# Kernel optimization log

Measured on AMD Instinct MI355X. Metric: run time of the kernel, lower is better.

Reference implementation:

```python
import jax, jax.numpy as jnp
import numpy as np

BANDWIDTH = 0.1
NUM_ITERS = 5


def setup_inputs() -> dict:
    key = jax.random.key(0)
    # image batch in [0,1], BCHW
    x = jax.random.uniform(key, (2, 3, 96, 96), dtype=jnp.float32)
    return {"x": x}


def reference(x):
    # Mean-shift filtering: each pixel feature y is iteratively moved to the
    # Gaussian-kernel weighted mean of ALL original pixel features:
    #   y_{t+1} = sum_j exp(-||y_t - x_j||^2 / (2 bw^2)) x_j / sum_j exp(...)
    B, C, H, W = x.shape
    N = H * W
    pts = x.reshape(B, C, N).transpose(0, 2, 1)  # [B, N, C] original points
    inv2bw2 = jnp.float32(1.0 / (2.0 * BANDWIDTH * BANDWIDTH))
    x_sq = jnp.sum(pts * pts, axis=-1)  # [B, N]

    def step(y, _):
        # squared pairwise distances via ||y||^2 + ||x||^2 - 2 y.x  -> [B, N, N]
        y_sq = jnp.sum(y * y, axis=-1)  # [B, N]
        d2 = y_sq[:, :, None] + x_sq[:, None, :] - 2.0 * jnp.einsum(
            'bnc,bmc->bnm', y, pts)
        w = jnp.exp(-jnp.maximum(d2, 0.0) * inv2bw2)  # Gaussian kernel weights
        num = jnp.einsum('bnm,bmc->bnc', w, pts)  # weighted sum of points
        den = jnp.sum(w, axis=-1, keepdims=True)  # normalizer (>= 1, self-weight)
        return num / den, None

    y, _ = jax.lax.scan(step, pts, None, length=NUM_ITERS)
    return y.transpose(0, 2, 1).reshape(B, C, H, W)
```

## Files before the change

kernel.cpp:

```cpp
#include <hip/hip_runtime.h>
#include <math.h>


typedef float v2f __attribute__((ext_vector_type(2)));

#define NPTS   9216
#define NB     2
#define TOT    (NB * NPTS)
#define MSPLIT 32
#define SLICE  (NPTS / MSPLIT)
#define WSLICE (SLICE / 4)
#define NPB    256
#define NTILES (NPTS / NPB)
#define LOG2E  1.44269504088896340736f

__device__ __forceinline__ v2f splat2(float v) { return (v2f){v, v}; }


__global__ __launch_bounds__(256, 4) void ms_iter(const float* __restrict__ x,
                                                  const float4* __restrict__ accIn,
                                                  float4* __restrict__ accOut,
                                                  float s, int first) {
    __shared__ float4 smem[1024];
    float* const xs = (float*)smem;
    float* const ys = xs + SLICE;
    float* const zs = ys + SLICE;
    float* const ws = zs + SLICE;
    float4* const ypar = smem + SLICE;
    float4* const red  = smem;

    const int tid  = threadIdx.x;
    const int lane = tid & 63;
    const int wv   = tid >> 6;
    const int k    = blockIdx.x % MSPLIT;
    const int tile = blockIdx.x / MSPLIT;
    const int b    = tile / NTILES;
    const int nt   = tile - b * NTILES;
    const int nbase = nt * NPB;
    const float* xb = x + b * 3 * NPTS;
    const int mbeg = k * SLICE;

    for (int i = tid; i < SLICE; i += 256) {
        int g = mbeg + i;
        float px = xb[g] * s;
        float py = xb[NPTS + g] * s;
        float pz = xb[2 * NPTS + g] * s;
        xs[i] = 2.f * px;
        ys[i] = 2.f * py;
        zs[i] = 2.f * pz;
        ws[i] = -fmaf(px, px, fmaf(py, py, pz * pz));
    }
    {
        float y0, y1, y2;
        if (first) {
            int n = nbase + tid;
            y0 = xb[n] * s; y1 = xb[NPTS + n] * s; y2 = xb[2 * NPTS + n] * s;
        } else {
            float4 a = accIn[b * NPTS + nbase + tid];
            float inv = 1.0f / a.w;
            y0 = a.x * inv; y1 = a.y * inv; y2 = a.z * inv;
        }
        ypar[tid] = make_float4(y0, y1, y2,
                                -fmaf(y0, y0, fmaf(y1, y1, y2 * y2)));
    }
    __syncthreads();

    v2f Yx[4], Yy[4], Yz[4], Yw[4], Ax[4], Ay[4], Az[4], Aw[4];
#pragma unroll
    for (int j = 0; j < 4; ++j) {
        float4 yp = ypar[lane + 64 * j];
        Yx[j] = splat2(yp.x); Yy[j] = splat2(yp.y);
        Yz[j] = splat2(yp.z); Yw[j] = splat2(yp.w);
        Ax[j] = splat2(0.f); Ay[j] = splat2(0.f);
        Az[j] = splat2(0.f); Aw[j] = splat2(0.f);
    }

    const float* xsw = xs + wv * WSLICE;
    const float* ysw = ys + wv * WSLICE;
    const float* zsw = zs + wv * WSLICE;
    const float* wsw = ws + wv * WSLICE;

    for (int i = 0; i < WSLICE; i += 8) {
#pragma unroll
        for (int half = 0; half < 2; ++half) {
            const int o = i + 4 * half;
            float4 PX = *(const float4*)(xsw + o);
            float4 PY = *(const float4*)(ysw + o);
            float4 PZ = *(const float4*)(zsw + o);
            float4 PW = *(const float4*)(wsw + o);
            v2f px0 = (v2f){PX.x, PX.y}, px1 = (v2f){PX.z, PX.w};
            v2f py0 = (v2f){PY.x, PY.y}, py1 = (v2f){PY.z, PY.w};
            v2f pz0 = (v2f){PZ.x, PZ.y}, pz1 = (v2f){PZ.z, PZ.w};
            v2f pw0 = (v2f){PW.x, PW.y}, pw1 = (v2f){PW.z, PW.w};
#pragma unroll
            for (int j = 0; j < 4; ++j) {
                v2f t0 = pw0 + Yw[j];
                t0 = __builtin_elementwise_fma(pz0, Yz[j], t0);
                t0 = __builtin_elementwise_fma(py0, Yy[j], t0);
                t0 = __builtin_elementwise_fma(px0, Yx[j], t0);
                v2f t1 = pw1 + Yw[j];
                t1 = __builtin_elementwise_fma(pz1, Yz[j], t1);
                t1 = __builtin_elementwise_fma(py1, Yy[j], t1);
                t1 = __builtin_elementwise_fma(px1, Yx[j], t1);
                v2f w0, w1;
                w0.x = __builtin_amdgcn_exp2f(t0.x);
                w0.y = __builtin_amdgcn_exp2f(t0.y);
                w1.x = __builtin_amdgcn_exp2f(t1.x);
                w1.y = __builtin_amdgcn_exp2f(t1.y);
                Ax[j] = __builtin_elementwise_fma(w0, px0, Ax[j]);
                Ay[j] = __builtin_elementwise_fma(w0, py0, Ay[j]);
                Az[j] = __builtin_elementwise_fma(w0, pz0, Az[j]);
                Aw[j] += w0;
                Ax[j] = __builtin_elementwise_fma(w1, px1, Ax[j]);
                Ay[j] = __builtin_elementwise_fma(w1, py1, Ay[j]);
                Az[j] = __builtin_elementwise_fma(w1, pz1, Az[j]);
                Aw[j] += w1;
            }
        }
    }

    __syncthreads();
#pragma unroll
    for (int j = 0; j < 4; ++j) {
        red[wv * NPB + lane + 64 * j] =
            make_float4(Ax[j].x + Ax[j].y, Ay[j].x + Ay[j].y,
                        Az[j].x + Az[j].y, Aw[j].x + Aw[j].y);
    }
    __syncthreads();
    {
        float4 r0 = red[tid];
        float4 r1 = red[NPB + tid];
        float4 r2 = red[2 * NPB + tid];
        float4 r3 = red[3 * NPB + tid];
        float ox = 0.5f * ((r0.x + r1.x) + (r2.x + r3.x));
        float oy = 0.5f * ((r0.y + r1.y) + (r2.y + r3.y));
        float oz = 0.5f * ((r0.z + r1.z) + (r2.z + r3.z));
        float od = (r0.w + r1.w) + (r2.w + r3.w);
        float* dst = (float*)&accOut[b * NPTS + nbase + tid];
        atomicAdd(dst + 0, ox);
        atomicAdd(dst + 1, oy);
        atomicAdd(dst + 2, oz);
        atomicAdd(dst + 3, od);
    }
}

__global__ __launch_bounds__(256) void ms_pack(const float4* __restrict__ acc4,
                                               float* __restrict__ out,
                                               float invs) {
    int gid = blockIdx.x * 256 + threadIdx.x;
    int b = gid / NPTS;
    int n = gid - b * NPTS;
    float4 a = acc4[gid];
    float f = invs / a.w;
    float* ob = out + b * 3 * NPTS;
    ob[n]            = a.x * f;
    ob[NPTS + n]     = a.y * f;
    ob[2 * NPTS + n] = a.z * f;
}

extern "C" void kernel_launch(void* const* d_in, const int* in_sizes, int n_in,
                              void* d_out, int out_size, void* d_ws, size_t ws_size,
                              hipStream_t stream) {
    const float* x = (const float*)d_in[0];
    float* out = (float*)d_out;
    float s = sqrtf(50.0f * LOG2E);

    float4* acc = (float4*)d_ws;

    hipMemsetAsync(acc, 0, (size_t)5 * TOT * sizeof(float4), stream);

    for (int it = 0; it < 5; ++it) {
        const float4* accIn = (it == 0) ? nullptr : acc + (size_t)(it - 1) * TOT;
        ms_iter<<<NB * NTILES * MSPLIT, 256, 0, stream>>>(
            x, accIn, acc + (size_t)it * TOT, s, it == 0 ? 1 : 0);
    }
    ms_pack<<<TOT / 256, 256, 0, stream>>>(acc + (size_t)4 * TOT, out, 1.0f / s);
}
```

Baseline: 235.0 us.

## Compute pairwise distance logits with split-bf16 MFMA instead of scalar FMAs

The pairwise dot products plus norm terms are moved onto the 32x32x16 bf16 MFMA. Each feature is split into hi and lo bf16 parts so the products keep close to fp32 accuracy. A new pre-pass kernel packs the point features into bf16 layout and float4 points once, and each wave streams points from global memory instead of staging them in LDS. The exp and weighted accumulation stay on the vector ALU, and the result is reduced across half-waves with a shuffle before the atomics. The risk is precision loss from the bf16 splitting, and the kernel now relies more on global memory and cache bandwidth.

```diff
diff --git a/kernel.cpp b/kernel.cpp
--- a/kernel.cpp
+++ b/kernel.cpp
@@ -2,145 +2,154 @@
 #include <math.h>
 
 
+#define NPTS 9216
+#define NB 2
+#define TOT (NB * NPTS)
+#define NTIL 288
+#define TPW 18
+#define LOG2E 1.44269504088896340736f
+
 typedef float v2f __attribute__((ext_vector_type(2)));
+typedef short bf16x8 __attribute__((ext_vector_type(8)));
+typedef float f32x16 __attribute__((ext_vector_type(16)));
 
-#define NPTS   9216
-#define NB     2
-#define TOT    (NB * NPTS)
-#define MSPLIT 32
-#define SLICE  (NPTS / MSPLIT)
-#define WSLICE (SLICE / 4)
-#define NPB    256
-#define NTILES (NPTS / NPB)
-#define LOG2E  1.44269504088896340736f
+__device__ __forceinline__ unsigned short bf16r(float x) {
+    unsigned u = __float_as_uint(x);
+    return (unsigned short)((u + 0x7fffu + ((u >> 16) & 1u)) >> 16);
+}
+__device__ __forceinline__ float bf16f(unsigned short h) {
+    return __uint_as_float((unsigned)h << 16);
+}
 
-__device__ __forceinline__ v2f splat2(float v) { return (v2f){v, v}; }
+__global__ __launch_bounds__(256) void ms_feat(const float* __restrict__ x,
+                                               short* __restrict__ pfeat,
+                                               float4* __restrict__ pts4,
+                                               float s) {
+    int gid = blockIdx.x * 256 + threadIdx.x;
+    int b = gid / NPTS, m = gid - b * NPTS;
+    const float* xb = x + b * 3 * NPTS;
+    float p0 = xb[m] * s, p1 = xb[NPTS + m] * s, p2 = xb[2 * NPTS + m] * s;
+    float np = -fmaf(p0, p0, fmaf(p1, p1, p2 * p2));
+    float a0 = 2.f * p0, a1 = 2.f * p1, a2 = 2.f * p2;
+    unsigned short Ah0 = bf16r(a0), Ah1 = bf16r(a1), Ah2 = bf16r(a2);
+    unsigned short Al0 = bf16r(a0 - bf16f(Ah0));
+    unsigned short Al1 = bf16r(a1 - bf16f(Ah1));
+    unsigned short Al2 = bf16r(a2 - bf16f(Ah2));
+    unsigned short Nh = bf16r(np);
+    unsigned short Nl = bf16r(np - bf16f(Nh));
+    uint4* dst = (uint4*)(pfeat + (size_t)gid * 16);
+    dst[0] = make_uint4((unsigned)Ah0 | ((unsigned)Ah1 << 16),
+                        (unsigned)Ah2 | ((unsigned)Ah0 << 16),
+                        (unsigned)Ah1 | ((unsigned)Ah2 << 16),
+                        (unsigned)Al0 | ((unsigned)Al1 << 16));
+    dst[1] = make_uint4((unsigned)Al2 | ((unsigned)Al0 << 16),
+                        (unsigned)Al1 | ((unsigned)Al2 << 16),
+                        (unsigned)Nh  | ((unsigned)Nl  << 16), 0u);
+    pts4[gid] = make_float4(p0, p1, p2, 1.0f);
+}
 
+__global__ __launch_bounds__(256, 4) void ms_iter(
+    const float* __restrict__ x, const float4* __restrict__ accIn,
+    float4* __restrict__ accOut, const short* __restrict__ pfeat,
+    const float4* __restrict__ pts4, float s, int first) {
 
-__global__ __launch_bounds__(256, 4) void ms_iter(const float* __restrict__ x,
-                                                  const float4* __restrict__ accIn,
-                                                  float4* __restrict__ accOut,
-                                                  float s, int first) {
-    __shared__ float4 smem[1024];
-    float* const xs = (float*)smem;
-    float* const ys = xs + SLICE;
-    float* const zs = ys + SLICE;
-    float* const ws = zs + SLICE;
-    float4* const ypar = smem + SLICE;
-    float4* const red  = smem;
+    const int tid = threadIdx.x;
+    const int l   = tid & 63;
+    const int wv  = tid >> 6;
+    const int col = l & 31;
+    const int hi  = l >> 5;
 
-    const int tid  = threadIdx.x;
-    const int lane = tid & 63;
-    const int wv   = tid >> 6;
-    const int k    = blockIdx.x % MSPLIT;
-    const int tile = blockIdx.x / MSPLIT;
-    const int b    = tile / NTILES;
-    const int nt   = tile - b * NTILES;
-    const int nbase = nt * NPB;
-    const float* xb = x + b * 3 * NPTS;
-    const int mbeg = k * SLICE;
+    int bid = blockIdx.x;
+    const int b  = bid / (4 * NTIL);
+    int r        = bid - b * 4 * NTIL;
+    const int nt = r >> 2;
+    const int mc = r & 3;
+    const int n  = nt * 32 + col;
+    const int t0 = (mc * 4 + wv) * TPW;
 
-    for (int i = tid; i < SLICE; i += 256) {
-        int g = mbeg + i;
-        float px = xb[g] * s;
-        float py = xb[NPTS + g] * s;
-        float pz = xb[2 * NPTS + g] * s;
-        xs[i] = 2.f * px;
-        ys[i] = 2.f * py;
-        zs[i] = 2.f * pz;
-        ws[i] = -fmaf(px, px, fmaf(py, py, pz * pz));
+    float y0, y1, y2;
+    if (first) {
+        const float* xb = x + b * 3 * NPTS;
+        y0 = xb[n] * s; y1 = xb[NPTS + n] * s; y2 = xb[2 * NPTS + n] * s;
+    } else {
+        float4 a = accIn[b * NPTS + n];
+        float inv = 1.0f / a.w;
+        y0 = a.x * inv; y1 = a.y * inv; y2 = a.z * inv;
     }
-    {
-        float y0, y1, y2;
-        if (first) {
-            int n = nbase + tid;
-            y0 = xb[n] * s; y1 = xb[NPTS + n] * s; y2 = xb[2 * NPTS + n] * s;
-        } else {
-            float4 a = accIn[b * NPTS + nbase + tid];
-            float inv = 1.0f / a.w;
-            y0 = a.x * inv; y1 = a.y * inv; y2 = a.z * inv;
-        }
-        ypar[tid] = make_float4(y0, y1, y2,
-                                -fmaf(y0, y0, fmaf(y1, y1, y2 * y2)));
-    }
-    __syncthreads();
-
-    v2f Yx[4], Yy[4], Yz[4], Yw[4], Ax[4], Ay[4], Az[4], Aw[4];
-#pragma unroll
-    for (int j = 0; j < 4; ++j) {
-        float4 yp = ypar[lane + 64 * j];
-        Yx[j] = splat2(yp.x); Yy[j] = splat2(yp.y);
-        Yz[j] = splat2(yp.z); Yw[j] = splat2(yp.w);
-        Ax[j] = splat2(0.f); Ay[j] = splat2(0.f);
-        Az[j] = splat2(0.f); Aw[j] = splat2(0.f);
+    float ny = -fmaf(y0, y0, fmaf(y1, y1, y2 * y2));
+    unsigned short Yh0 = bf16r(y0), Yh1 = bf16r(y1), Yh2 = bf16r(y2);
+    unsigned short Yl0 = bf16r(y0 - bf16f(Yh0));
+    unsigned short Yl1 = bf16r(y1 - bf16f(Yh1));
+    unsigned short Yl2 = bf16r(y2 - bf16f(Yh2));
+    union { unsigned w[4]; bf16x8 v; } yf;
+    if (hi == 0) {
+        yf.w[0] = (unsigned)Yh0 | ((unsigned)Yh1 << 16);
+        yf.w[1] = (unsigned)Yh2 | ((unsigned)Yl0 << 16);
+        yf.w[2] = (unsigned)Yl1 | ((unsigned)Yl2 << 16);
+        yf.w[3] = (unsigned)Yh0 | ((unsigned)Yh1 << 16);
+    } else {
+        yf.w[0] = (unsigned)Yh2 | ((unsigned)Yl0 << 16);
+        yf.w[1] = (unsigned)Yl1 | ((unsigned)Yl2 << 16);
+        yf.w[2] = 0x3F803F80u;
+        yf.w[3] = 0u;
     }
 
-    const float* xsw = xs + wv * WSLICE;
-    const float* ysw = ys + wv * WSLICE;
-    const float* zsw = zs + wv * WSLICE;
-    const float* wsw = ws + wv * WSLICE;
+    f32x16 cin;
+#pragma unroll
+    for (int i = 0; i < 16; ++i) cin[i] = ny;
 
-    for (int i = 0; i < WSLICE; i += 8) {
+    v2f Axy = (v2f){0.f, 0.f};
+    v2f Azw = (v2f){0.f, 0.f};
+
+    const short*  pfb = pfeat + (size_t)b * NPTS * 16;
+    const float4* pbb = pts4 + (size_t)b * NPTS + 4 * hi;
+
+#pragma unroll 2
+    for (int t = t0; t < t0 + TPW; ++t) {
+        const int m0 = t * 32;
+        bf16x8 pf = *(const bf16x8*)(pfb + (size_t)(m0 + col) * 16 + 8 * hi);
+        f32x16 u = __builtin_amdgcn_mfma_f32_32x32x16_bf16(pf, yf.v, cin,
+                                                           0, 0, 0);
+        const float4* pb = pbb + m0;
 #pragma unroll
-        for (int half = 0; half < 2; ++half) {
-            const int o = i + 4 * half;
-            float4 PX = *(const float4*)(xsw + o);
-            float4 PY = *(const float4*)(ysw + o);
-            float4 PZ = *(const float4*)(zsw + o);
-            float4 PW = *(const float4*)(wsw + o);
-            v2f px0 = (v2f){PX.x, PX.y}, px1 = (v2f){PX.z, PX.w};
-            v2f py0 = (v2f){PY.x, PY.y}, py1 = (v2f){PY.z, PY.w};
-            v2f pz0 = (v2f){PZ.x, PZ.y}, pz1 = (v2f){PZ.z, PZ.w};
-            v2f pw0 = (v2f){PW.x, PW.y}, pw1 = (v2f){PW.z, PW.w};
-#pragma unroll
-            for (int j = 0; j < 4; ++j) {
-                v2f t0 = pw0 + Yw[j];
-                t0 = __builtin_elementwise_fma(pz0, Yz[j], t0);
-                t0 = __builtin_elementwise_fma(py0, Yy[j], t0);
-                t0 = __builtin_elementwise_fma(px0, Yx[j], t0);
-                v2f t1 = pw1 + Yw[j];
-                t1 = __builtin_elementwise_fma(pz1, Yz[j], t1);
-                t1 = __builtin_elementwise_fma(py1, Yy[j], t1);
-                t1 = __builtin_elementwise_fma(px1, Yx[j], t1);
-                v2f w0, w1;
-                w0.x = __builtin_amdgcn_exp2f(t0.x);
-                w0.y = __builtin_amdgcn_exp2f(t0.y);
-                w1.x = __builtin_amdgcn_exp2f(t1.x);
-                w1.y = __builtin_amdgcn_exp2f(t1.y);
-                Ax[j] = __builtin_elementwise_fma(w0, px0, Ax[j]);
-                Ay[j] = __builtin_elementwise_fma(w0, py0, Ay[j]);
-                Az[j] = __builtin_elementwise_fma(w0, pz0, Az[j]);
-                Aw[j] += w0;
-                Ax[j] = __builtin_elementwise_fma(w1, px1, Ax[j]);
-                Ay[j] = __builtin_elementwise_fma(w1, py1, Ay[j]);
-                Az[j] = __builtin_elementwise_fma(w1, pz1, Az[j]);
-                Aw[j] += w1;
-            }
+        for (int q = 0; q < 4; ++q) {
+            float4 P0 = pb[8 * q + 0];
+            float4 P1 = pb[8 * q + 1];
+            float4 P2 = pb[8 * q + 2];
+            float4 P3 = pb[8 * q + 3];
+            float w0 = __builtin_amdgcn_exp2f(u[4 * q + 0]);
+            float w1 = __builtin_amdgcn_exp2f(u[4 * q + 1]);
+            float w2 = __builtin_amdgcn_exp2f(u[4 * q + 2]);
+            float w3 = __builtin_amdgcn_exp2f(u[4 * q + 3]);
+            Axy = __builtin_elementwise_fma((v2f){w0, w0},
+                                            (v2f){P0.x, P0.y}, Axy);
+            Azw = __builtin_elementwise_fma((v2f){w0, w0},
+                                            (v2f){P0.z, P0.w}, Azw);
+            Axy = __builtin_elementwise_fma((v2f){w1, w1},
+                                            (v2f){P1.x, P1.y}, Axy);
+            Azw = __builtin_elementwise_fma((v2f){w1, w1},
+                                            (v2f){P1.z, P1.w}, Azw);
+            Axy = __builtin_elementwise_fma((v2f){w2, w2},
+                                            (v2f){P2.x, P2.y}, Axy);
+            Azw = __builtin_elementwise_fma((v2f){w2, w2},
+                                            (v2f){P2.z, P2.w}, Azw);
+            Axy = __builtin_elementwise_fma((v2f){w3, w3},
+                                            (v2f){P3.x, P3.y}, Axy);
+            Azw = __builtin_elementwise_fma((v2f){w3, w3},
+                                            (v2f){P3.z, P3.w}, Azw);
         }
     }
 
-    __syncthreads();
-#pragma unroll
-    for (int j = 0; j < 4; ++j) {
-        red[wv * NPB + lane + 64 * j] =
-            make_float4(Ax[j].x + Ax[j].y, Ay[j].x + Ay[j].y,
-                        Az[j].x + Az[j].y, Aw[j].x + Aw[j].y);
-    }
-    __syncthreads();
-    {
-        float4 r0 = red[tid];
-        float4 r1 = red[NPB + tid];
-        float4 r2 = red[2 * NPB + tid];
-        float4 r3 = red[3 * NPB + tid];
-        float ox = 0.5f * ((r0.x + r1.x) + (r2.x + r3.x));
-        float oy = 0.5f * ((r0.y + r1.y) + (r2.y + r3.y));
-        float oz = 0.5f * ((r0.z + r1.z) + (r2.z + r3.z));
-        float od = (r0.w + r1.w) + (r2.w + r3.w);
-        float* dst = (float*)&accOut[b * NPTS + nbase + tid];
-        atomicAdd(dst + 0, ox);
-        atomicAdd(dst + 1, oy);
-        atomicAdd(dst + 2, oz);
-        atomicAdd(dst + 3, od);
+    float hx = __shfl(Axy[0], col + 32);
+    float hy = __shfl(Axy[1], col + 32);
+    float hz = __shfl(Azw[0], col + 32);
+    float hd = __shfl(Azw[1], col + 32);
+    if (l < 32) {
+        float* dst = (float*)&accOut[b * NPTS + n];
+        atomicAdd(dst + 0, Axy[0] + hx);
+        atomicAdd(dst + 1, Axy[1] + hy);
+        atomicAdd(dst + 2, Azw[0] + hz);
+        atomicAdd(dst + 3, Azw[1] + hd);
     }
 }
 
@@ -165,14 +174,17 @@
     float* out = (float*)d_out;
     float s = sqrtf(50.0f * LOG2E);
 
-    float4* acc = (float4*)d_ws;
+    float4* acc   = (float4*)d_ws;
+    short*  pfeat = (short*)(acc + (size_t)5 * TOT);
+    float4* pts4  = (float4*)(pfeat + (size_t)TOT * 16);
 
     hipMemsetAsync(acc, 0, (size_t)5 * TOT * sizeof(float4), stream);
+    ms_feat<<<TOT / 256, 256, 0, stream>>>(x, pfeat, pts4, s);
 
     for (int it = 0; it < 5; ++it) {
         const float4* accIn = (it == 0) ? nullptr : acc + (size_t)(it - 1) * TOT;
-        ms_iter<<<NB * NTILES * MSPLIT, 256, 0, stream>>>(
-            x, accIn, acc + (size_t)it * TOT, s, it == 0 ? 1 : 0);
+        ms_iter<<<NB * NTIL * 4, 256, 0, stream>>>(
+            x, accIn, acc + (size_t)it * TOT, pfeat, pts4, s, it == 0 ? 1 : 0);
     }
     ms_pack<<<TOT / 256, 256, 0, stream>>>(acc + (size_t)4 * TOT, out, 1.0f / s);
 }
```

New measurement: 501.7 us. 114% more time.
